# Optimization experiments

Measured on AMD Instinct MI355X. Metric: run time of the kernel, lower is better.

The kernel has to match this reference:

```python
import jax, jax.numpy as jnp
import numpy as np

N = 100000      # nodes
E = 3200000     # edges (avg degree 32)
F_IN = 512      # node features
H = 256         # hidden width (channels[0])
C = 64          # num_classes
K = 10          # APPNP steps
ALPHA = 0.1     # teleport prob


def setup_inputs() -> dict:
    key = jax.random.key(0)
    k1, k2, k3, k4 = jax.random.split(key, 4)
    x = jax.random.normal(k1, (N, F_IN), dtype=jnp.float32)
    edge_index = jax.random.randint(k2, (2, E), 0, N, dtype=jnp.int32)
    W1 = jax.random.normal(k3, (F_IN, H), dtype=jnp.float32) * (1.0 / np.sqrt(F_IN))
    b1 = jnp.zeros((H,), dtype=jnp.float32)
    W2 = jax.random.normal(k4, (H, C), dtype=jnp.float32) * (1.0 / np.sqrt(H))
    b2 = jnp.zeros((C,), dtype=jnp.float32)
    return {"x": x, "edge_index": edge_index, "W1": W1, "b1": b1, "W2": W2, "b2": b2}


def reference(x, edge_index, W1, b1, W2, b2):
    # MLP encoder (dropout is identity at eval time)
    h = jax.nn.relu(x @ W1 + b1) @ W2 + b2  # [N, C]

    # GCN normalization with added self-loops (PyG APPNP default)
    loops = jnp.arange(N, dtype=edge_index.dtype)
    row = jnp.concatenate([edge_index[0], loops])  # source
    col = jnp.concatenate([edge_index[1], loops])  # target
    deg = jax.ops.segment_sum(jnp.ones_like(col, dtype=h.dtype), col, num_segments=N)
    dinv = jnp.where(deg > 0, jax.lax.rsqrt(deg), 0.0)
    norm = (dinv[row] * dinv[col])[:, None]  # [E+N, 1]

    # APPNP: z_{k+1} = (1-alpha) * A_hat z_k + alpha * h
    z = h
    for _ in range(K):
        msg = z[row] * norm                                   # gather + scale
        agg = jax.ops.segment_sum(msg, col, num_segments=N)   # scatter-add
        z = (1.0 - ALPHA) * agg + ALPHA * h

    return jax.nn.log_softmax(z, axis=1)
```

## Files before the change

kernel.cpp:

```cpp
#include <hip/hip_runtime.h>
#include <hip/hip_bf16.h>

#define F_IN 512
#define H_DIM 256
#define C_DIM 64
#define K_STEPS 10
#define ALPHA 0.1f

typedef __attribute__((ext_vector_type(8))) short bf16x8;
typedef __attribute__((ext_vector_type(4))) float f32x4;

static __device__ __forceinline__ ushort f2bf(float f) {
    __hip_bfloat16 b = __float2bfloat16(f);
    return *(ushort*)&b;
}
static __device__ __forceinline__ float bflo(unsigned int w) {
    union { unsigned int i; float f; } v; v.i = w << 16; return v.f;
}
static __device__ __forceinline__ float bfhi(unsigned int w) {
    union { unsigned int i; float f; } v; v.i = w & 0xffff0000u; return v.f;
}

#define ACC8(u) do { \
    acc[0] += bflo(u.x); acc[1] += bfhi(u.x); \
    acc[2] += bflo(u.y); acc[3] += bfhi(u.y); \
    acc[4] += bflo(u.z); acc[5] += bfhi(u.z); \
    acc[6] += bflo(u.w); acc[7] += bfhi(u.w); } while (0)

__global__ void prep_kernel(const float* __restrict__ W1, ushort* __restrict__ W1p,
                            const float* __restrict__ W2, ushort* __restrict__ W2p,
                            int* __restrict__ cnt, int n)
{
    const int o = blockIdx.x * 256 + threadIdx.x;
    {
        const int j = o & 7;
        const int l = (o >> 3) & 63;
        const int b = o >> 9;
        const int f = b & 15, ks = b >> 4;
        const int k = ks * 32 + (l >> 4) * 8 + j;
        const int col = f * 16 + (l & 15);
        W1p[o] = f2bf(W1[k * H_DIM + col]);
    }
    if (o < 16384) {
        const int j = o & 7;
        const int l = (o >> 3) & 63;
        const int b = o >> 9;
        const int f = b & 3, kk = b >> 2;
        const int k = kk * 32 + (l >> 4) * 8 + j;
        const int col = f * 16 + (l & 15);
        W2p[o] = f2bf(W2[k * C_DIM + col]);
    }
    if (o < n) cnt[o] = 0;
}

__global__ void rank_kernel(const int* __restrict__ col, int* __restrict__ cnt,
                            int* __restrict__ rank, int e)
{
    int i = blockIdx.x * 256 + threadIdx.x;
    if (i < e) rank[i] = atomicAdd(&cnt[col[i]], 1);
}

__global__ __launch_bounds__(256) void scan1_kernel(
    const int* __restrict__ cnt, int* __restrict__ rowptr, int* __restrict__ sums,
    float* __restrict__ dinv, int n)
{
    __shared__ int lds[256];
    const int t = threadIdx.x;
    const int base = blockIdx.x * 1024 + t * 4;
    int v[4];
    #pragma unroll
    for (int j = 0; j < 4; ++j) v[j] = (base + j < n) ? cnt[base + j] : 0;
    const int tsum = v[0] + v[1] + v[2] + v[3];
    lds[t] = tsum;
    __syncthreads();
    for (int o = 1; o < 256; o <<= 1) {
        const int add = (t >= o) ? lds[t - o] : 0;
        __syncthreads();
        lds[t] += add;
        __syncthreads();
    }
    int run = lds[t] - tsum;
    #pragma unroll
    for (int j = 0; j < 4; ++j) {
        if (base + j < n) {
            rowptr[base + j] = run;
            dinv[base + j] = rsqrtf((float)v[j] + 1.0f);
        }
        run += v[j];
    }
    if (t == 255) sums[blockIdx.x] = lds[255];
}

__global__ __launch_bounds__(128) void scan2_kernel(int* __restrict__ sums, int nc)
{
    __shared__ int lds[128];
    const int t = threadIdx.x;
    const int v = (t < nc) ? sums[t] : 0;
    lds[t] = v;
    __syncthreads();
    for (int o = 1; o < 128; o <<= 1) {
        const int add = (t >= o) ? lds[t - o] : 0;
        __syncthreads();
        lds[t] += add;
        __syncthreads();
    }
    if (t < nc) sums[t] = lds[t] - v;
}

__global__ void scan3_kernel(int* __restrict__ rowptr, const int* __restrict__ sums, int n, int e)
{
    int i = blockIdx.x * 256 + threadIdx.x;
    if (i < n) rowptr[i] += sums[i >> 10];
    else if (i == n) rowptr[n] = e;
}

__global__ void fill_kernel(const int* __restrict__ row, const int* __restrict__ col,
                            const int* __restrict__ rowptr, const int* __restrict__ rank,
                            int* __restrict__ csr_src, int e)
{
    int i = blockIdx.x * 256 + threadIdx.x;
    if (i < e) csr_src[rowptr[col[i]] + rank[i]] = row[i];
}

__global__ __launch_bounds__(256) void mlp_mfma_kernel(
    const float* __restrict__ x,
    const ushort* __restrict__ W1p, const float* __restrict__ b1,
    const ushort* __restrict__ W2p, const float* __restrict__ b2,
    const float* __restrict__ dinv,
    float* __restrict__ h, ushort* __restrict__ zs, int n)
{
    __shared__ __align__(16) short h1s[4][16 * 264];

    const int t = threadIdx.x;
    const int lane = t & 63;
    const int wv = t >> 6;
    const int ln15 = lane & 15;
    const int hi = lane >> 4;
    const long row0 = (long)blockIdx.x * 64 + wv * 16;

    long arow = row0 + ln15;
    if (arow > (long)n - 1) arow = n - 1;
    const float* xrow = x + arow * F_IN;

    f32x4 acc[16];
    #pragma unroll
    for (int f = 0; f < 16; ++f) acc[f] = (f32x4){0.f, 0.f, 0.f, 0.f};

    for (int ks = 0; ks < 16; ++ks) {
        const float4 a0 = *(const float4*)&xrow[ks * 32 + hi * 8];
        const float4 a1 = *(const float4*)&xrow[ks * 32 + hi * 8 + 4];
        bf16x8 af;
        af[0] = (short)f2bf(a0.x); af[1] = (short)f2bf(a0.y);
        af[2] = (short)f2bf(a0.z); af[3] = (short)f2bf(a0.w);
        af[4] = (short)f2bf(a1.x); af[5] = (short)f2bf(a1.y);
        af[6] = (short)f2bf(a1.z); af[7] = (short)f2bf(a1.w);
        const ushort* wb = W1p + (long)ks * 8192 + lane * 8;
        #pragma unroll
        for (int f = 0; f < 16; ++f) {
            const bf16x8 bfv = *(const bf16x8*)(wb + f * 512);
            acc[f] = __builtin_amdgcn_mfma_f32_16x16x32_bf16(af, bfv, acc[f], 0, 0, 0);
        }
    }

    short* hb = h1s[wv];
    #pragma unroll
    for (int f = 0; f < 16; ++f) {
        const int col = f * 16 + ln15;
        const float bias = b1[col];
        #pragma unroll
        for (int v = 0; v < 4; ++v) {
            float val = acc[f][v] + bias;
            val = val > 0.f ? val : 0.f;
            hb[(hi * 4 + v) * 264 + col] = (short)f2bf(val);
        }
    }

    f32x4 acc2[4];
    #pragma unroll
    for (int f = 0; f < 4; ++f) acc2[f] = (f32x4){0.f, 0.f, 0.f, 0.f};
    #pragma unroll
    for (int kk = 0; kk < 8; ++kk) {
        const bf16x8 a2 = *(const bf16x8*)&hb[ln15 * 264 + kk * 32 + hi * 8];
        #pragma unroll
        for (int f = 0; f < 4; ++f) {
            const bf16x8 b2f = *(const bf16x8*)&W2p[(kk * 4 + f) * 512 + lane * 8];
            acc2[f] = __builtin_amdgcn_mfma_f32_16x16x32_bf16(a2, b2f, acc2[f], 0, 0, 0);
        }
    }

    float di4[4];
    #pragma unroll
    for (int v = 0; v < 4; ++v) {
        const long r = row0 + hi * 4 + v;
        di4[v] = (r < n) ? dinv[r] : 0.f;
    }
    #pragma unroll
    for (int f = 0; f < 4; ++f) {
        const int col = f * 16 + ln15;
        const float bias = b2[col];
        #pragma unroll
        for (int v = 0; v < 4; ++v) {
            const long r = row0 + hi * 4 + v;
            if (r < n) {
                const float val = acc2[f][v] + bias;
                h[r * C_DIM + col] = val;
                zs[r * C_DIM + col] = f2bf(val * di4[v]);
            }
        }
    }
}

__global__ __launch_bounds__(256) void gather8_kernel(
    const int* __restrict__ rowptr, const int* __restrict__ csr_src,
    const float* __restrict__ dinv, const float* __restrict__ hbuf,
    const ushort* __restrict__ zs_in, ushort* __restrict__ zs_out,
    float* __restrict__ out, int n, int final_it)
{
    const int node = (blockIdx.x * 256 + threadIdx.x) >> 6;
    if (node >= n) return;
    const int lane = threadIdx.x & 63;
    const int s = lane >> 3;
    const int cg = lane & 7;

    const int p0 = rowptr[node];
    const int p1 = rowptr[node + 1];

    float acc[8];
    #pragma unroll
    for (int c = 0; c < 8; ++c) acc[c] = 0.f;

    if (s == 0) {
        const uint4 u = *(const uint4*)&zs_in[(long)node * C_DIM + cg * 8];
        ACC8(u);
    }

    int p = p0 + s;
    for (; p + 8 < p1; p += 16) {
        const int i0 = csr_src[p];
        const int i1 = csr_src[p + 8];
        const uint4 u0 = *(const uint4*)&zs_in[(long)i0 * C_DIM + cg * 8];
        const uint4 u1 = *(const uint4*)&zs_in[(long)i1 * C_DIM + cg * 8];
        ACC8(u0);
        ACC8(u1);
    }
    if (p < p1) {
        const int i0 = csr_src[p];
        const uint4 u0 = *(const uint4*)&zs_in[(long)i0 * C_DIM + cg * 8];
        ACC8(u0);
    }

    #pragma unroll
    for (int c = 0; c < 8; ++c) {
        acc[c] += __shfl_xor(acc[c], 8, 64);
        acc[c] += __shfl_xor(acc[c], 16, 64);
        acc[c] += __shfl_xor(acc[c], 32, 64);
    }

    if (s == 0) {
        const float di = dinv[node];
        const long off = (long)node * C_DIM + cg * 8;
        const float4 ha = *(const float4*)&hbuf[off];
        const float4 hb = *(const float4*)&hbuf[off + 4];
        float z[8];
        z[0] = (1.0f - ALPHA) * (di * acc[0]) + ALPHA * ha.x;
        z[1] = (1.0f - ALPHA) * (di * acc[1]) + ALPHA * ha.y;
        z[2] = (1.0f - ALPHA) * (di * acc[2]) + ALPHA * ha.z;
        z[3] = (1.0f - ALPHA) * (di * acc[3]) + ALPHA * ha.w;
        z[4] = (1.0f - ALPHA) * (di * acc[4]) + ALPHA * hb.x;
        z[5] = (1.0f - ALPHA) * (di * acc[5]) + ALPHA * hb.y;
        z[6] = (1.0f - ALPHA) * (di * acc[6]) + ALPHA * hb.z;
        z[7] = (1.0f - ALPHA) * (di * acc[7]) + ALPHA * hb.w;
        if (!final_it) {
            uint4 o;
            o.x = ((unsigned)f2bf(z[1] * di) << 16) | f2bf(z[0] * di);
            o.y = ((unsigned)f2bf(z[3] * di) << 16) | f2bf(z[2] * di);
            o.z = ((unsigned)f2bf(z[5] * di) << 16) | f2bf(z[4] * di);
            o.w = ((unsigned)f2bf(z[7] * di) << 16) | f2bf(z[6] * di);
            *(uint4*)&zs_out[off] = o;
        } else {
            float m = z[0];
            #pragma unroll
            for (int j = 1; j < 8; ++j) m = fmaxf(m, z[j]);
            m = fmaxf(m, __shfl_xor(m, 1, 64));
            m = fmaxf(m, __shfl_xor(m, 2, 64));
            m = fmaxf(m, __shfl_xor(m, 4, 64));
            float se = 0.f;
            #pragma unroll
            for (int j = 0; j < 8; ++j) se += expf(z[j] - m);
            se += __shfl_xor(se, 1, 64);
            se += __shfl_xor(se, 2, 64);
            se += __shfl_xor(se, 4, 64);
            const float ls = m + logf(se);
            *(float4*)&out[off]     = make_float4(z[0] - ls, z[1] - ls, z[2] - ls, z[3] - ls);
            *(float4*)&out[off + 4] = make_float4(z[4] - ls, z[5] - ls, z[6] - ls, z[7] - ls);
        }
    }
}

extern "C" void kernel_launch(void* const* d_in, const int* in_sizes, int n_in,
                              void* d_out, int out_size, void* d_ws, size_t ws_size,
                              hipStream_t stream)
{
    const float* x  = (const float*)d_in[0];
    const int* ei   = (const int*)d_in[1];
    const float* W1 = (const float*)d_in[2];
    const float* b1 = (const float*)d_in[3];
    const float* W2 = (const float*)d_in[4];
    const float* b2 = (const float*)d_in[5];
    float* out = (float*)d_out;

    const int N = in_sizes[0] / F_IN;
    const int E = in_sizes[1] / 2;
    const int* row = ei;
    const int* col = ei + E;

    float*  h      = (float*)d_ws;
    ushort* zs_a   = (ushort*)(h + (long)N * C_DIM);
    ushort* zs_b   = zs_a + (long)N * C_DIM;
    float*  dinv   = (float*)(zs_b + (long)N * C_DIM);
    int*    cnt    = (int*)(dinv + N);
    int*    rowptr = cnt + N;
    int*    rank   = rowptr + N + 16;
    int*    csr_src = rank + E;
    int*    sums   = csr_src + E;
    ushort* W1p    = (ushort*)(sums + 128);
    ushort* W2p    = W1p + 131072;

    const int eblk = (E + 255) / 256;
    const int nchunks = (N + 1023) / 1024;

    prep_kernel<<<512, 256, 0, stream>>>(W1, W1p, W2, W2p, cnt, N);

    rank_kernel<<<eblk, 256, 0, stream>>>(col, cnt, rank, E);
    scan1_kernel<<<nchunks, 256, 0, stream>>>(cnt, rowptr, sums, dinv, N);
    scan2_kernel<<<1, 128, 0, stream>>>(sums, nchunks);
    scan3_kernel<<<(N + 256) / 256, 256, 0, stream>>>(rowptr, sums, N, E);
    fill_kernel<<<eblk, 256, 0, stream>>>(row, col, rowptr, rank, csr_src, E);

    mlp_mfma_kernel<<<(N + 63) / 64, 256, 0, stream>>>(x, W1p, b1, W2p, b2,
                                                       dinv, h, zs_a, N);

    const int gblk = (N + 3) / 4;
    for (int it = 0; it < K_STEPS; ++it) {
        const ushort* in = (it & 1) ? zs_b : zs_a;
        ushort* outb     = (it & 1) ? zs_a : zs_b;
        gather8_kernel<<<gblk, 256, 0, stream>>>(rowptr, csr_src, dinv, h,
                                                 in, outb, out, N,
                                                 it == K_STEPS - 1 ? 1 : 0);
    }
}
```

Measured before the change: 947.5 us.

## Slice features into 16-column planes for gather, stage W1 via LDS, vectorize CSR build

After: 2.112 ms. 2.23x slower.

```diff
diff --git a/kernel.cpp b/kernel.cpp
--- a/kernel.cpp
+++ b/kernel.cpp
@@ -21,11 +21,9 @@
     union { unsigned int i; float f; } v; v.i = w & 0xffff0000u; return v.f;
 }
 
-#define ACC8(u) do { \
-    acc[0] += bflo(u.x); acc[1] += bfhi(u.x); \
-    acc[2] += bflo(u.y); acc[3] += bfhi(u.y); \
-    acc[4] += bflo(u.z); acc[5] += bfhi(u.z); \
-    acc[6] += bflo(u.w); acc[7] += bfhi(u.w); } while (0)
+#define GLOAD_LDS16(gp, lp) __builtin_amdgcn_global_load_lds( \
+    (const __attribute__((address_space(1))) unsigned int*)(gp), \
+    (__attribute__((address_space(3))) unsigned int*)(lp), 16, 0, 0)
 
 __global__ void prep_kernel(const float* __restrict__ W1, ushort* __restrict__ W1p,
                             const float* __restrict__ W2, ushort* __restrict__ W2p,
@@ -56,8 +54,17 @@
 __global__ void rank_kernel(const int* __restrict__ col, int* __restrict__ cnt,
                             int* __restrict__ rank, int e)
 {
-    int i = blockIdx.x * 256 + threadIdx.x;
-    if (i < e) rank[i] = atomicAdd(&cnt[col[i]], 1);
+    const int i0 = (blockIdx.x * 256 + threadIdx.x) * 4;
+    if (i0 + 3 < e) {
+        const int4 c = *(const int4*)&col[i0];
+        const int r0 = atomicAdd(&cnt[c.x], 1);
+        const int r1 = atomicAdd(&cnt[c.y], 1);
+        const int r2 = atomicAdd(&cnt[c.z], 1);
+        const int r3 = atomicAdd(&cnt[c.w], 1);
+        *(int4*)&rank[i0] = make_int4(r0, r1, r2, r3);
+    } else {
+        for (int i = i0; i < e; ++i) rank[i] = atomicAdd(&cnt[col[i]], 1);
+    }
 }
 
 __global__ __launch_bounds__(256) void scan1_kernel(
@@ -118,8 +125,18 @@
                             const int* __restrict__ rowptr, const int* __restrict__ rank,
                             int* __restrict__ csr_src, int e)
 {
-    int i = blockIdx.x * 256 + threadIdx.x;
-    if (i < e) csr_src[rowptr[col[i]] + rank[i]] = row[i];
+    const int i0 = (blockIdx.x * 256 + threadIdx.x) * 4;
+    if (i0 + 3 < e) {
+        const int4 c  = *(const int4*)&col[i0];
+        const int4 rk = *(const int4*)&rank[i0];
+        const int4 rw = *(const int4*)&row[i0];
+        csr_src[rowptr[c.x] + rk.x] = rw.x;
+        csr_src[rowptr[c.y] + rk.y] = rw.y;
+        csr_src[rowptr[c.z] + rk.z] = rw.z;
+        csr_src[rowptr[c.w] + rk.w] = rw.w;
+    } else {
+        for (int i = i0; i < e; ++i) csr_src[rowptr[col[i]] + rank[i]] = row[i];
+    }
 }
 
 __global__ __launch_bounds__(256) void mlp_mfma_kernel(
@@ -127,9 +144,9 @@
     const ushort* __restrict__ W1p, const float* __restrict__ b1,
     const ushort* __restrict__ W2p, const float* __restrict__ b2,
     const float* __restrict__ dinv,
-    float* __restrict__ h, ushort* __restrict__ zs, int n)
-{
-    __shared__ __align__(16) short h1s[4][16 * 264];
+    ushort* __restrict__ ah_sl, ushort* __restrict__ zs_sl, int n)
+{
+    __shared__ __align__(16) char smem[32768];
 
     const int t = threadIdx.x;
     const int lane = t & 63;
@@ -140,38 +157,59 @@
 
     long arow = row0 + ln15;
     if (arow > (long)n - 1) arow = n - 1;
-    const float* xrow = x + arow * F_IN;
+    const float4* xp = (const float4*)(x + arow * F_IN);
 
     f32x4 acc[16];
     #pragma unroll
     for (int f = 0; f < 16; ++f) acc[f] = (f32x4){0.f, 0.f, 0.f, 0.f};
 
+    {
+        const char* g = (const char*)(W1p);
+        char* l = smem;
+        #pragma unroll
+        for (int j = 0; j < 4; ++j)
+            GLOAD_LDS16(g + j * 4096 + wv * 1024 + lane * 16,
+                        l + j * 4096 + wv * 1024);
+    }
+    __syncthreads();
+
     for (int ks = 0; ks < 16; ++ks) {
-        const float4 a0 = *(const float4*)&xrow[ks * 32 + hi * 8];
-        const float4 a1 = *(const float4*)&xrow[ks * 32 + hi * 8 + 4];
+        if (ks < 15) {
+            const char* g = (const char*)(W1p + (size_t)(ks + 1) * 8192);
+            char* l = smem + ((ks + 1) & 1) * 16384;
+            #pragma unroll
+            for (int j = 0; j < 4; ++j)
+                GLOAD_LDS16(g + j * 4096 + wv * 1024 + lane * 16,
+                            l + j * 4096 + wv * 1024);
+        }
+        const float4 a0 = xp[ks * 8 + hi * 2];
+        const float4 a1 = xp[ks * 8 + hi * 2 + 1];
         bf16x8 af;
         af[0] = (short)f2bf(a0.x); af[1] = (short)f2bf(a0.y);
         af[2] = (short)f2bf(a0.z); af[3] = (short)f2bf(a0.w);
         af[4] = (short)f2bf(a1.x); af[5] = (short)f2bf(a1.y);
         af[6] = (short)f2bf(a1.z); af[7] = (short)f2bf(a1.w);
-        const ushort* wb = W1p + (long)ks * 8192 + lane * 8;
+        const ushort* wb = (const ushort*)(smem + (ks & 1) * 16384) + lane * 8;
         #pragma unroll
         for (int f = 0; f < 16; ++f) {
             const bf16x8 bfv = *(const bf16x8*)(wb + f * 512);
             acc[f] = __builtin_amdgcn_mfma_f32_16x16x32_bf16(af, bfv, acc[f], 0, 0, 0);
         }
-    }
-
-    short* hb = h1s[wv];
+        __syncthreads();
+    }
+
+    char* hreg = smem + wv * 8192;
     #pragma unroll
     for (int f = 0; f < 16; ++f) {
         const int col = f * 16 + ln15;
         const float bias = b1[col];
         #pragma unroll
         for (int v = 0; v < 4; ++v) {
+            const int r = hi * 4 + v;
             float val = acc[f][v] + bias;
             val = val > 0.f ? val : 0.f;
-            hb[(hi * 4 + v) * 264 + col] = (short)f2bf(val);
+            const int pos = (r * 256 + col) * 2;
+            *(short*)(hreg + (pos ^ ((r & 7) << 4))) = (short)f2bf(val);
         }
     }
 
@@ -180,7 +218,8 @@
     for (int f = 0; f < 4; ++f) acc2[f] = (f32x4){0.f, 0.f, 0.f, 0.f};
     #pragma unroll
     for (int kk = 0; kk < 8; ++kk) {
-        const bf16x8 a2 = *(const bf16x8*)&hb[ln15 * 264 + kk * 32 + hi * 8];
+        const int pos = (ln15 * 256 + kk * 32 + hi * 8) * 2;
+        const bf16x8 a2 = *(const bf16x8*)(hreg + (pos ^ ((ln15 & 7) << 4)));
         #pragma unroll
         for (int f = 0; f < 4; ++f) {
             const bf16x8 b2f = *(const bf16x8*)&W2p[(kk * 4 + f) * 512 + lane * 8];
@@ -203,98 +242,87 @@
             const long r = row0 + hi * 4 + v;
             if (r < n) {
                 const float val = acc2[f][v] + bias;
-                h[r * C_DIM + col] = val;
-                zs[r * C_DIM + col] = f2bf(val * di4[v]);
+                ah_sl[(size_t)f * n * 16 + r * 16 + ln15] = f2bf(ALPHA * val);
+                zs_sl[(size_t)f * n * 16 + r * 16 + ln15] = f2bf(val * di4[v]);
             }
         }
     }
 }
 
-__global__ __launch_bounds__(256) void gather8_kernel(
+__global__ __launch_bounds__(256) void gather_sl_kernel(
     const int* __restrict__ rowptr, const int* __restrict__ csr_src,
-    const float* __restrict__ dinv, const float* __restrict__ hbuf,
-    const ushort* __restrict__ zs_in, ushort* __restrict__ zs_out,
-    float* __restrict__ out, int n, int final_it)
-{
-    const int node = (blockIdx.x * 256 + threadIdx.x) >> 6;
+    const float* __restrict__ dinv, const ushort* __restrict__ ah_sl,
+    const ushort* __restrict__ zin, ushort* __restrict__ zout,
+    float* __restrict__ zfin, int n, int final_it)
+{
+    const int b = blockIdx.x;
+    const int sg = (b & 7) >> 1;
+    const int q = ((b >> 3) << 1) | (b & 1);
+    const int node = q * 4 + (threadIdx.x >> 6);
     if (node >= n) return;
     const int lane = threadIdx.x & 63;
-    const int s = lane >> 3;
-    const int cg = lane & 7;
+    const int s = lane >> 2;
+    const int c4 = lane & 3;
+    const size_t sbase = (size_t)sg * n * 16;
 
     const int p0 = rowptr[node];
     const int p1 = rowptr[node + 1];
 
-    float acc[8];
-    #pragma unroll
-    for (int c = 0; c < 8; ++c) acc[c] = 0.f;
-
+    float a0 = 0.f, a1 = 0.f, a2 = 0.f, a3 = 0.f;
     if (s == 0) {
-        const uint4 u = *(const uint4*)&zs_in[(long)node * C_DIM + cg * 8];
-        ACC8(u);
-    }
-
-    int p = p0 + s;
-    for (; p + 8 < p1; p += 16) {
-        const int i0 = csr_src[p];
-        const int i1 = csr_src[p + 8];
-        const uint4 u0 = *(const uint4*)&zs_in[(long)i0 * C_DIM + cg * 8];
-        const uint4 u1 = *(const uint4*)&zs_in[(long)i1 * C_DIM + cg * 8];
-        ACC8(u0);
-        ACC8(u1);
-    }
-    if (p < p1) {
-        const int i0 = csr_src[p];
-        const uint4 u0 = *(const uint4*)&zs_in[(long)i0 * C_DIM + cg * 8];
-        ACC8(u0);
-    }
-
-    #pragma unroll
-    for (int c = 0; c < 8; ++c) {
-        acc[c] += __shfl_xor(acc[c], 8, 64);
-        acc[c] += __shfl_xor(acc[c], 16, 64);
-        acc[c] += __shfl_xor(acc[c], 32, 64);
-    }
-
-    if (s == 0) {
+        const uint2 u = *(const uint2*)&zin[sbase + (size_t)node * 16 + c4 * 4];
+        a0 += bflo(u.x); a1 += bfhi(u.x); a2 += bflo(u.y); a3 += bfhi(u.y);
+    }
+    for (int p = p0 + s; p < p1; p += 16) {
+        const int idx = __builtin_nontemporal_load(&csr_src[p]);
+        const uint2 u = *(const uint2*)&zin[sbase + (size_t)idx * 16 + c4 * 4];
+        a0 += bflo(u.x); a1 += bfhi(u.x); a2 += bflo(u.y); a3 += bfhi(u.y);
+    }
+
+    #pragma unroll
+    for (int o = 4; o < 64; o <<= 1) {
+        a0 += __shfl_xor(a0, o, 64);
+        a1 += __shfl_xor(a1, o, 64);
+        a2 += __shfl_xor(a2, o, 64);
+        a3 += __shfl_xor(a3, o, 64);
+    }
+
+    if (lane < 4) {
         const float di = dinv[node];
-        const long off = (long)node * C_DIM + cg * 8;
-        const float4 ha = *(const float4*)&hbuf[off];
-        const float4 hb = *(const float4*)&hbuf[off + 4];
-        float z[8];
-        z[0] = (1.0f - ALPHA) * (di * acc[0]) + ALPHA * ha.x;
-        z[1] = (1.0f - ALPHA) * (di * acc[1]) + ALPHA * ha.y;
-        z[2] = (1.0f - ALPHA) * (di * acc[2]) + ALPHA * ha.z;
-        z[3] = (1.0f - ALPHA) * (di * acc[3]) + ALPHA * ha.w;
-        z[4] = (1.0f - ALPHA) * (di * acc[4]) + ALPHA * hb.x;
-        z[5] = (1.0f - ALPHA) * (di * acc[5]) + ALPHA * hb.y;
-        z[6] = (1.0f - ALPHA) * (di * acc[6]) + ALPHA * hb.z;
-        z[7] = (1.0f - ALPHA) * (di * acc[7]) + ALPHA * hb.w;
+        const float w = (1.0f - ALPHA) * di;
+        const uint2 ua = *(const uint2*)&ah_sl[sbase + (size_t)node * 16 + c4 * 4];
+        const float z0 = w * a0 + bflo(ua.x);
+        const float z1 = w * a1 + bfhi(ua.x);
+        const float z2 = w * a2 + bflo(ua.y);
+        const float z3 = w * a3 + bfhi(ua.y);
         if (!final_it) {
-            uint4 o;
-            o.x = ((unsigned)f2bf(z[1] * di) << 16) | f2bf(z[0] * di);
-            o.y = ((unsigned)f2bf(z[3] * di) << 16) | f2bf(z[2] * di);
-            o.z = ((unsigned)f2bf(z[5] * di) << 16) | f2bf(z[4] * di);
-            o.w = ((unsigned)f2bf(z[7] * di) << 16) | f2bf(z[6] * di);
-            *(uint4*)&zs_out[off] = o;
+            uint2 o2;
+            o2.x = ((unsigned)f2bf(z1 * di) << 16) | f2bf(z0 * di);
+            o2.y = ((unsigned)f2bf(z3 * di) << 16) | f2bf(z2 * di);
+            *(uint2*)&zout[sbase + (size_t)node * 16 + c4 * 4] = o2;
         } else {
-            float m = z[0];
-            #pragma unroll
-            for (int j = 1; j < 8; ++j) m = fmaxf(m, z[j]);
-            m = fmaxf(m, __shfl_xor(m, 1, 64));
-            m = fmaxf(m, __shfl_xor(m, 2, 64));
-            m = fmaxf(m, __shfl_xor(m, 4, 64));
-            float se = 0.f;
-            #pragma unroll
-            for (int j = 0; j < 8; ++j) se += expf(z[j] - m);
-            se += __shfl_xor(se, 1, 64);
-            se += __shfl_xor(se, 2, 64);
-            se += __shfl_xor(se, 4, 64);
-            const float ls = m + logf(se);
-            *(float4*)&out[off]     = make_float4(z[0] - ls, z[1] - ls, z[2] - ls, z[3] - ls);
-            *(float4*)&out[off + 4] = make_float4(z[4] - ls, z[5] - ls, z[6] - ls, z[7] - ls);
-        }
-    }
+            *(float4*)&zfin[sbase + (size_t)node * 16 + c4 * 4] =
+                make_float4(z0, z1, z2, z3);
+        }
+    }
+}
+
+__global__ __launch_bounds__(256) void lsm_kernel(
+    const float* __restrict__ zfin, float* __restrict__ out, int n)
+{
+    const int gid = blockIdx.x * 256 + threadIdx.x;
+    const int node = gid >> 6;
+    if (node >= n) return;
+    const int lane = threadIdx.x & 63;
+    const float v = zfin[(size_t)(lane >> 4) * n * 16 + (size_t)node * 16 + (lane & 15)];
+    float m = v;
+    #pragma unroll
+    for (int o = 32; o > 0; o >>= 1) m = fmaxf(m, __shfl_xor(m, o, 64));
+    const float ex = expf(v - m);
+    float s = ex;
+    #pragma unroll
+    for (int o = 32; o > 0; o >>= 1) s += __shfl_xor(s, o, 64);
+    out[(size_t)node * C_DIM + lane] = v - m - logf(s);
 }
 
 extern "C" void kernel_launch(void* const* d_in, const int* in_sizes, int n_in,
@@ -314,10 +342,11 @@
     const int* row = ei;
     const int* col = ei + E;
 
-    float*  h      = (float*)d_ws;
-    ushort* zs_a   = (ushort*)(h + (long)N * C_DIM);
-    ushort* zs_b   = zs_a + (long)N * C_DIM;
-    float*  dinv   = (float*)(zs_b + (long)N * C_DIM);
+    ushort* ah_sl  = (ushort*)d_ws;
+    ushort* zs_a   = ah_sl + (size_t)N * C_DIM;
+    ushort* zs_b   = zs_a + (size_t)N * C_DIM;
+    float*  zfin   = (float*)(zs_b + (size_t)N * C_DIM);
+    float*  dinv   = zfin + (size_t)N * C_DIM;
     int*    cnt    = (int*)(dinv + N);
     int*    rowptr = cnt + N;
     int*    rank   = rowptr + N + 16;
@@ -326,26 +355,29 @@
     ushort* W1p    = (ushort*)(sums + 128);
     ushort* W2p    = W1p + 131072;
 
-    const int eblk = (E + 255) / 256;
+    const int eblk4 = (E / 4 + 255) / 256;
     const int nchunks = (N + 1023) / 1024;
 
     prep_kernel<<<512, 256, 0, stream>>>(W1, W1p, W2, W2p, cnt, N);
 
-    rank_kernel<<<eblk, 256, 0, stream>>>(col, cnt, rank, E);
+    rank_kernel<<<eblk4, 256, 0, stream>>>(col, cnt, rank, E);
     scan1_kernel<<<nchunks, 256, 0, stream>>>(cnt, rowptr, sums, dinv, N);
     scan2_kernel<<<1, 128, 0, stream>>>(sums, nchunks);
     scan3_kernel<<<(N + 256) / 256, 256, 0, stream>>>(rowptr, sums, N, E);
-    fill_kernel<<<eblk, 256, 0, stream>>>(row, col, rowptr, rank, csr_src, E);
+    fill_kernel<<<eblk4, 256, 0, stream>>>(row, col, rowptr, rank, csr_src, E);
 
     mlp_mfma_kernel<<<(N + 63) / 64, 256, 0, stream>>>(x, W1p, b1, W2p, b2,
-                                                       dinv, h, zs_a, N);
-
-    const int gblk = (N + 3) / 4;
+                                                       dinv, ah_sl, zs_a, N);
+
+    const int pairs = ((N + 3) / 4 + 1) / 2;
+    const int gblocks = pairs * 8;
     for (int it = 0; it < K_STEPS; ++it) {
         const ushort* in = (it & 1) ? zs_b : zs_a;
         ushort* outb     = (it & 1) ? zs_a : zs_b;
-        gather8_kernel<<<gblk, 256, 0, stream>>>(rowptr, csr_src, dinv, h,
-                                                 in, outb, out, N,
-                                                 it == K_STEPS - 1 ? 1 : 0);
-    }
-}
+        gather_sl_kernel<<<gblocks, 256, 0, stream>>>(rowptr, csr_src, dinv, ah_sl,
+                                                      in, outb, zfin, N,
+                                                      it == K_STEPS - 1 ? 1 : 0);
+    }
+
+    lsm_kernel<<<(N * C_DIM + 255) / 256, 256, 0, stream>>>(zfin, out, N);
+}
```
